# Performance work log

Measured on AMD Instinct MI355X. Metric: run time of the kernel, lower is better.

Reference implementation:

```python
import jax, jax.numpy as jnp
import numpy as np

SQRT2 = 1.4142135623730951
MH_C = 0.8673250705840776  # (2/sqrt(3)) * pi**(-1/4), mexican-hat normalizer


def _bn(x, eps=1e-5):
    # BatchNorm (training-mode batch stats, default affine gamma=1, beta=0)
    mu = jnp.mean(x, axis=0, keepdims=True)
    var = jnp.var(x, axis=0, keepdims=True)
    return (x - mu) / jnp.sqrt(var + eps)


def setup_inputs() -> dict:
    key = jax.random.key(0)
    ks = jax.random.split(key, 10)
    N, F, E, B, OUT = 1024, 1024, 32768, 16, 10
    H = F // 2  # 512 after Haar DWT
    x = jax.random.normal(ks[0], (N, F), dtype=jnp.float32)
    edge_index = jax.random.randint(ks[1], (2, E), 0, N, dtype=jnp.int32)
    batch = jnp.sort(jax.random.randint(ks[2], (N,), 0, B, dtype=jnp.int32))
    w_att = jax.random.normal(ks[3], (2,), dtype=jnp.float32)  # Linear(2,1,bias=False)
    wk_scale = jnp.ones((H, H), dtype=jnp.float32)
    wk_trans = jax.random.normal(ks[4], (H, H), dtype=jnp.float32) * 0.1
    wk_wav_w = jax.random.normal(ks[5], (H, H), dtype=jnp.float32) * 0.05
    wk_base_w = jax.random.normal(ks[6], (H, H), dtype=jnp.float32) * 0.05
    fc1_w = jax.random.normal(ks[7], (512, F + H), dtype=jnp.float32) * 0.02
    fc1_b = jnp.zeros((512,), dtype=jnp.float32)
    fc2_w = jax.random.normal(ks[8], (OUT, 512), dtype=jnp.float32) * 0.02
    fc2_b = jnp.zeros((OUT,), dtype=jnp.float32)
    return {"x": x, "w_att": w_att, "wk_scale": wk_scale, "wk_trans": wk_trans,
            "wk_wav_w": wk_wav_w, "wk_base_w": wk_base_w, "fc1_w": fc1_w,
            "fc1_b": fc1_b, "fc2_w": fc2_w, "fc2_b": fc2_b,
            "edge_index": edge_index, "batch": batch, "num_graphs": B}


def reference(x, w_att, wk_scale, wk_trans, wk_wav_w, wk_base_w,
              fc1_w, fc1_b, fc2_w, fc2_b, edge_index, batch, num_graphs):
    N = x.shape[0]
    # --- WaveletAttention: Haar ('db1') DWT over the feature dim ---
    xe, xo = x[:, 0::2], x[:, 1::2]
    low = (xe + xo) / SQRT2            # [N, 512]
    high = (xe - xo) / SQRT2           # [N, 512]
    scores = jax.nn.sigmoid(low * w_att[0] + high * w_att[1])
    h = scores * low + (1.0 - scores) * high
    # --- GINConv aggregation (eps=0): self + sum of neighbor features ---
    src, dst = edge_index[0], edge_index[1]
    agg = h + jax.ops.segment_sum(h[src], dst, num_segments=N)  # [N, 512]
    # --- WavKAN layer 512->512 (mexican hat) ---
    xs = (agg[:, None, :] - wk_trans) / wk_scale                # [N, 512, 512]
    xs2 = xs * xs
    mh = MH_C * (1.0 - xs2) * jnp.exp(-0.5 * xs2)
    wav = jnp.einsum('noi,oi->no', mh, wk_wav_w)                # [N, 512]
    base = jax.nn.silu(agg) @ wk_base_w.T
    conv_out = _bn(wav + base)   # WavKAN-internal BatchNorm1d
    conv_out = _bn(conv_out)     # bn1 (dropout p=0 -> identity)
    # --- skip concat + bn2 ---
    z = _bn(jnp.concatenate([x, conv_out], axis=1))             # [N, 1536]
    # --- global mean pool over graphs ---
    sums = jax.ops.segment_sum(z, batch, num_segments=num_graphs)
    cnts = jax.ops.segment_sum(jnp.ones((N,), z.dtype), batch, num_segments=num_graphs)
    pooled = sums / jnp.maximum(cnts, 1.0)[:, None]             # [B, 1536]
    # --- classifier head (eval-mode dropout = identity) ---
    h1 = jax.nn.relu(pooled @ fc1_w.T + fc1_b)
    return h1 @ fc2_w.T + fc2_b
```

## Files before the change

kernel.cpp:

```cpp
#include <hip/hip_runtime.h>
#include <math.h>

#define N_NODES 1024
#define F_DIM   1024
#define H_DIM   512
#define E_EDGES 32768
#define B_GRAPHS 16
#define OUT_DIM 10
#define FH_DIM  1536
#define EPS 1e-5f
#define MH_C_D 0.8673250705840776
#define C2_D   0.72134752044448170368
#define C2_F   ((float)C2_D)
#define CSC    0.84932180028801904272f
#define WC2F   ((float)(MH_C_D / C2_D))
#define INV_SQRT2 0.70710678118654752440f

typedef float v2f __attribute__((ext_vector_type(2)));
typedef unsigned int u32;
typedef const __attribute__((address_space(1))) u32 gu32;
typedef __attribute__((address_space(3))) u32 lu32;

#if __has_builtin(__builtin_amdgcn_exp2f)
#define EXP2NEG(x) __builtin_amdgcn_exp2f(-(x))
#else
#define EXP2NEG(x) __expf(-0.69314718055994530942f * (x))
#endif

__global__ __launch_bounds__(256) void k_setup(const float* __restrict__ x,
                                               const float* __restrict__ watt,
                                               float* __restrict__ h,
                                               const float* __restrict__ scale,
                                               const float* __restrict__ trans,
                                               const float* __restrict__ ww,
                                               const float* __restrict__ bw,
                                               float* __restrict__ pk,
                                               float* __restrict__ zbase) {
    const int bid = blockIdx.x;
    const int t = threadIdx.x;
    if (bid < 2048) {
        int idx = bid * 256 + t;
        float2 p = ((const float2*)x)[idx];
        float lo = (p.x + p.y) * INV_SQRT2;
        float hi = (p.x - p.y) * INV_SQRT2;
        float tt = lo * watt[0] + hi * watt[1];
        float sc = 1.0f / (1.0f + __expf(-tt));
        h[idx] = sc * lo + (1.0f - sc) * hi;
    } else if (bid < 3072) {
        int g = (bid - 2048) * 256 + t;
        float iv = 1.0f / scale[g];
        float4 p;
        p.x = iv * CSC;
        p.y = trans[g] * iv * CSC;
        p.z = ww[g] * WC2F;
        p.w = bw[g];
        ((float4*)pk)[g] = p;
    } else {
        zbase[(bid - 3072) * 256 + t] = 0.0f;
    }
}

__global__ __launch_bounds__(256) void k_hx(const int* __restrict__ dst,
                                            int* __restrict__ deg,
                                            const float* __restrict__ x,
                                            float* __restrict__ xsum,
                                            float* __restrict__ xsum2) {
    const int bid = blockIdx.x;
    const int t = threadIdx.x;
    if (bid < 128) {
        int e = bid * 256 + t;
        atomicAdd(&deg[dst[e]], 1);
    } else {
        const int n0 = (bid - 128) * 16;
        float s[4] = {}, s2[4] = {};
        for (int r = 0; r < 16; ++r) {
            #pragma unroll
            for (int ch = 0; ch < 4; ++ch) {
                float v = x[(n0 + r) * F_DIM + ch * 256 + t];
                s[ch] += v; s2[ch] += v * v;
            }
        }
        #pragma unroll
        for (int ch = 0; ch < 4; ++ch) {
            unsafeAtomicAdd(&xsum[ch * 256 + t], s[ch]);
            unsafeAtomicAdd(&xsum2[ch * 256 + t], s2[ch]);
        }
    }
}

__global__ __launch_bounds__(1024) void k_scan(const int* __restrict__ deg,
                                               int* __restrict__ start,
                                               int* __restrict__ cursor) {
    __shared__ int wsum[16];
    int t = threadIdx.x;
    int lane = t & 63, wid = t >> 6;
    int v = deg[t];
    int x = v;
    #pragma unroll
    for (int off = 1; off < 64; off <<= 1) {
        int y = __shfl_up(x, off, 64);
        if (lane >= off) x += y;
    }
    if (lane == 63) wsum[wid] = x;
    __syncthreads();
    if (t < 16) {
        int w = wsum[t];
        int xs = w;
        #pragma unroll
        for (int off = 1; off < 16; off <<= 1) {
            int y = __shfl_up(xs, off, 64);
            if (t >= off) xs += y;
        }
        wsum[t] = xs - w;
    }
    __syncthreads();
    int excl = wsum[wid] + x - v;
    start[t] = excl;
    cursor[t] = excl;
}

__global__ __launch_bounds__(256) void k_fill(const int* __restrict__ src,
                                              const int* __restrict__ dst,
                                              int* __restrict__ cursor,
                                              int* __restrict__ elist) {
    int e = blockIdx.x * 256 + threadIdx.x;
    int slot = atomicAdd(&cursor[dst[e]], 1);
    elist[slot] = src[e];
}

__global__ __launch_bounds__(256) void k_gather(const float* __restrict__ h,
                                                const int* __restrict__ start,
                                                const int* __restrict__ deg,
                                                const int* __restrict__ elist,
                                                float* __restrict__ agg) {
    int d = blockIdx.x;
    int t = threadIdx.x;
    int st = start[d], dg = deg[d];
    const float2* h2 = (const float2*)h;
    float2 a = h2[d * 256 + t];
    int k = 0;
    for (; k + 4 <= dg; k += 4) {
        int s0 = elist[st + k];
        int s1 = elist[st + k + 1];
        int s2 = elist[st + k + 2];
        int s3 = elist[st + k + 3];
        float2 v0 = h2[s0 * 256 + t];
        float2 v1 = h2[s1 * 256 + t];
        float2 v2 = h2[s2 * 256 + t];
        float2 v3 = h2[s3 * 256 + t];
        a.x += (v0.x + v1.x) + (v2.x + v3.x);
        a.y += (v0.y + v1.y) + (v2.y + v3.y);
    }
    for (; k < dg; ++k) {
        int s0 = elist[st + k];
        float2 v0 = h2[s0 * 256 + t];
        a.x += v0.x; a.y += v0.y;
    }
    ((float2*)agg)[d * 256 + t] = a;
}

__global__ __launch_bounds__(256) void k_transpose(const float* __restrict__ agg,
                                                   float* __restrict__ aggT,
                                                   float* __restrict__ siluT) {
    __shared__ float tile[64 * 65];
    const int t = threadIdx.x;
    const int n0 = blockIdx.x * 64;
    const int i0 = blockIdx.y * 64;
    #pragma unroll
    for (int v = 0; v < 4; ++v) {
        int flat = v * 256 + t;
        int r = flat >> 4, c4 = flat & 15;
        float4 a = *(const float4*)&agg[(n0 + r) * H_DIM + i0 + c4 * 4];
        tile[(c4 * 4 + 0) * 65 + r] = a.x;
        tile[(c4 * 4 + 1) * 65 + r] = a.y;
        tile[(c4 * 4 + 2) * 65 + r] = a.z;
        tile[(c4 * 4 + 3) * 65 + r] = a.w;
    }
    __syncthreads();
    #pragma unroll
    for (int v = 0; v < 4; ++v) {
        int flat = v * 256 + t;
        int il = flat >> 4, c4 = flat & 15;
        float4 a;
        a.x = tile[il * 65 + c4 * 4 + 0];
        a.y = tile[il * 65 + c4 * 4 + 1];
        a.z = tile[il * 65 + c4 * 4 + 2];
        a.w = tile[il * 65 + c4 * 4 + 3];
        int g = (i0 + il) * N_NODES + n0 + c4 * 4;
        *(float4*)&aggT[g] = a;
        float4 s;
        s.x = a.x / (1.0f + __expf(-a.x));
        s.y = a.y / (1.0f + __expf(-a.y));
        s.z = a.z / (1.0f + __expf(-a.z));
        s.w = a.w / (1.0f + __expf(-a.w));
        *(float4*)&siluT[g] = s;
    }
}

#define TN 64
#define TO 64
#define KI 16
#define TOP (TO + 1)
#define ZSPLIT 8
#define ZLEN (H_DIM / ZSPLIT)
__global__ __launch_bounds__(256) void k_wavelet(const float* __restrict__ aggT,
                                                 const float* __restrict__ siluT,
                                                 const float* __restrict__ pk,
                                                 float* __restrict__ vbp) {
    __shared__ float sA[KI * TN];
    __shared__ float sS[KI * TN];
    __shared__ float4 sP4[KI * TOP];

    const int t  = threadIdx.x;
    const int n0 = blockIdx.x * TN;
    const int o0 = blockIdx.y * TO;
    const int z0 = blockIdx.z * ZLEN;
    const int nl = (t & 15) * 4;
    const int ol = (t >> 4) * 4;

    v2f accw[4][2] = {};
    v2f accb[4][2] = {};

    for (int stg = 0; stg < ZLEN / KI; ++stg) {
        const int i0 = z0 + stg * KI;
        __syncthreads();
        {
            int g = (i0 + (t >> 4)) * N_NODES + n0 + nl;
            __builtin_amdgcn_global_load_lds((gu32*)&aggT[g],  (lu32*)&sA[t * 4], 16, 0, 0);
            __builtin_amdgcn_global_load_lds((gu32*)&siluT[g], (lu32*)&sS[t * 4], 16, 0, 0);
        }
        #pragma unroll
        for (int j = 0; j < 4; ++j) {
            int u = j * 256 + t;
            int o = u >> 4, ii = u & 15;
            sP4[ii * TOP + o] = ((const float4*)pk)[(o0 + o) * H_DIM + i0 + ii];
        }
        __syncthreads();
        #pragma unroll 4
        for (int ii = 0; ii < KI; ++ii) {
            float4 a = *(const float4*)&sA[ii * TN + nl];
            float4 s = *(const float4*)&sS[ii * TN + nl];
            v2f a01 = {a.x, a.y}, a23 = {a.z, a.w};
            v2f s01 = {s.x, s.y}, s23 = {s.z, s.w};
            #pragma unroll
            for (int oo = 0; oo < 4; ++oo) {
                float4 p = sP4[ii * TOP + ol + oo];
                float wcs = p.z * C2_F;
                v2f iv2 = {p.x, p.x};
                v2f tf2 = {p.y, p.y};
                v2f w2  = {p.z, p.z};
                v2f wc2 = {wcs, wcs};
                v2f b2  = {p.w, p.w};
                {
                    v2f y  = a01 * iv2 - tf2;
                    v2f y2 = y * y;
                    v2f e; e.x = EXP2NEG(y2.x); e.y = EXP2NEG(y2.y);
                    v2f wm = wc2 - w2 * y2;
                    accw[oo][0] += wm * e;
                    accb[oo][0] += s01 * b2;
                }
                {
                    v2f y  = a23 * iv2 - tf2;
                    v2f y2 = y * y;
                    v2f e; e.x = EXP2NEG(y2.x); e.y = EXP2NEG(y2.y);
                    v2f wm = wc2 - w2 * y2;
                    accw[oo][1] += wm * e;
                    accb[oo][1] += s23 * b2;
                }
            }
        }
    }
    float* out = vbp + (size_t)blockIdx.z * (N_NODES * H_DIM);
    #pragma unroll
    for (int nn = 0; nn < 4; ++nn) {
        int pr = nn >> 1, cmu = nn & 1;
        float4 o4;
        o4.x = cmu ? accw[0][pr].y + accb[0][pr].y : accw[0][pr].x + accb[0][pr].x;
        o4.y = cmu ? accw[1][pr].y + accb[1][pr].y : accw[1][pr].x + accb[1][pr].x;
        o4.z = cmu ? accw[2][pr].y + accb[2][pr].y : accw[2][pr].x + accb[2][pr].x;
        o4.w = cmu ? accw[3][pr].y + accb[3][pr].y : accw[3][pr].x + accb[3][pr].x;
        *(float4*)&out[(n0 + nl + nn) * H_DIM + o0 + ol] = o4;
    }
}

__global__ __launch_bounds__(256) void k_reduce(const float* __restrict__ vbp,
                                                float* __restrict__ vb,
                                                float* __restrict__ colsum,
                                                float* __restrict__ colsum2) {
    const int b = blockIdx.x;
    const int o0 = (b & 7) * 64;
    const int n0 = (b >> 3) * 64;
    const int t = threadIdx.x;
    const int oc = o0 + (t & 63);
    const int nsub = t >> 6;
    float s = 0.f, s2 = 0.f;
    for (int r = 0; r < 16; ++r) {
        int n = n0 + r * 4 + nsub;
        size_t idx = (size_t)n * H_DIM + oc;
        float v = 0.f;
        #pragma unroll
        for (int z = 0; z < ZSPLIT; ++z) v += vbp[z * (N_NODES * H_DIM) + idx];
        vb[idx] = v;
        s += v; s2 += v * v;
    }
    __shared__ float sh1[256], sh2[256];
    sh1[t] = s; sh2[t] = s2;
    __syncthreads();
    if (t < 64) {
        s  = sh1[t] + sh1[t + 64] + sh1[t + 128] + sh1[t + 192];
        s2 = sh2[t] + sh2[t + 64] + sh2[t + 128] + sh2[t + 192];
        unsafeAtomicAdd(&colsum[o0 + t], s);
        unsafeAtomicAdd(&colsum2[o0 + t], s2);
    }
}

__global__ __launch_bounds__(256) void k_pool(const float* __restrict__ x,
                                              const float* __restrict__ vb,
                                              const int* __restrict__ batch,
                                              const float* __restrict__ colsum,
                                              const float* __restrict__ colsum2,
                                              const float* __restrict__ xsum,
                                              const float* __restrict__ xsum2,
                                              float* __restrict__ pooled) {
    const int b = blockIdx.x;
    const int ch = blockIdx.y;
    const int t = threadIdx.x;

    __shared__ int s_cnt[4];
    __shared__ int s_st;
    int c = 0;
    for (int n = t; n < N_NODES; n += 256) {
        int bb = batch[n];
        int pb = (n == 0) ? -1 : batch[n - 1];
        c += (bb == b) ? 1 : 0;
        if (bb == b && pb != b) s_st = n;
    }
    #pragma unroll
    for (int off = 32; off > 0; off >>= 1) c += __shfl_down(c, off);
    if ((t & 63) == 0) s_cnt[t >> 6] = c;
    __syncthreads();
    int cnt = s_cnt[0] + s_cnt[1] + s_cnt[2] + s_cnt[3];
    int st = (cnt > 0) ? s_st : 0;
    float ic = (cnt > 0) ? 1.0f / (float)cnt : 0.f;

    float acc = 0.f;
    if (ch < 4) {
        int col = ch * 256 + t;
        float mu  = xsum[col] * (1.0f / N_NODES);
        float var = xsum2[col] * (1.0f / N_NODES) - mu * mu;
        if (var < 0.f) var = 0.f;
        float S = 1.0f / sqrtf(var + EPS);
        const float* base = x + col;
        for (int r = 0; r < cnt; ++r) acc += base[(size_t)(st + r) * F_DIM];
        pooled[b * FH_DIM + col] = (acc * ic - mu) * S;
    } else {
        int col = (ch - 4) * 256 + t;
        float mu  = colsum[col] * (1.0f / N_NODES);
        float var = colsum2[col] * (1.0f / N_NODES) - mu * mu;
        if (var < 0.f) var = 0.f;
        float s1v = 1.0f / sqrtf(var + EPS);
        float v1  = var * s1v * s1v;
        float s2v = 1.0f / sqrtf(v1 + EPS);
        float v2  = v1 * s2v * s2v;
        float s3v = 1.0f / sqrtf(v2 + EPS);
        float S = s1v * s2v * s3v;
        const float* base = vb + col;
        for (int r = 0; r < cnt; ++r) acc += base[(size_t)(st + r) * H_DIM];
        pooled[b * FH_DIM + F_DIM + col] = (acc * ic - mu) * S;
    }
}

__global__ __launch_bounds__(256) void k_fc1(const float* __restrict__ pooled,
                                             const float* __restrict__ w,
                                             const float* __restrict__ bias,
                                             float* __restrict__ h1) {
    int wid = (blockIdx.x * 256 + threadIdx.x) >> 6;
    int lane = threadIdx.x & 63;
    int b = wid >> 9, o = wid & 511;
    const float4* pr = (const float4*)(pooled + b * FH_DIM);
    const float4* wr = (const float4*)(w + o * FH_DIM);
    float acc = 0.f;
    #pragma unroll
    for (int k = 0; k < 6; ++k) {
        float4 a = pr[k * 64 + lane];
        float4 v = wr[k * 64 + lane];
        acc += a.x * v.x + a.y * v.y + a.z * v.z + a.w * v.w;
    }
    #pragma unroll
    for (int off = 32; off > 0; off >>= 1) acc += __shfl_down(acc, off);
    if (lane == 0) h1[b * H_DIM + o] = fmaxf(acc + bias[o], 0.f);
}

__global__ __launch_bounds__(256) void k_fc2(const float* __restrict__ h1,
                                             const float* __restrict__ w,
                                             const float* __restrict__ bias,
                                             float* __restrict__ outp) {
    int wid = (blockIdx.x * 256 + threadIdx.x) >> 6;
    int lane = threadIdx.x & 63;
    if (wid >= B_GRAPHS * OUT_DIM) return;
    int b = wid / OUT_DIM, u = wid % OUT_DIM;
    const float4* hr = (const float4*)(h1 + b * H_DIM);
    const float4* wr = (const float4*)(w + u * H_DIM);
    float acc = 0.f;
    #pragma unroll
    for (int k = 0; k < 2; ++k) {
        float4 a = hr[k * 64 + lane];
        float4 v = wr[k * 64 + lane];
        acc += a.x * v.x + a.y * v.y + a.z * v.z + a.w * v.w;
    }
    #pragma unroll
    for (int off = 32; off > 0; off >>= 1) acc += __shfl_down(acc, off);
    if (lane == 0) outp[b * OUT_DIM + u] = acc + bias[u];
}

extern "C" void kernel_launch(void* const* d_in, const int* in_sizes, int n_in,
                              void* d_out, int out_size, void* d_ws, size_t ws_size,
                              hipStream_t stream) {
    const float* x       = (const float*)d_in[0];
    const float* w_att   = (const float*)d_in[1];
    const float* wk_scale= (const float*)d_in[2];
    const float* wk_trans= (const float*)d_in[3];
    const float* wk_wav  = (const float*)d_in[4];
    const float* wk_base = (const float*)d_in[5];
    const float* fc1_w   = (const float*)d_in[6];
    const float* fc1_b   = (const float*)d_in[7];
    const float* fc2_w   = (const float*)d_in[8];
    const float* fc2_b   = (const float*)d_in[9];
    const int*   eidx    = (const int*)d_in[10];
    const int*   batch   = (const int*)d_in[11];
    float* outp = (float*)d_out;

    float* ws = (float*)d_ws;
    const int NH = N_NODES * H_DIM;
    float* h      = ws;
    float* agg    = h + NH;
    float* aggT   = agg + NH;
    float* siluT  = aggT + NH;
    float* pk     = siluT + NH;
    float* vbp    = pk + 4 * (H_DIM * H_DIM);
    float* vb     = vbp + (size_t)ZSPLIT * NH;
    float* colsum = vb + NH;
    float* colsum2= colsum + 512;
    float* xsum   = colsum2 + 512;
    float* xsum2  = xsum + 1024;
    int*   deg    = (int*)(xsum2 + 1024);
    int*   estart = deg + N_NODES;
    int*   cursor = estart + N_NODES;
    int*   elist  = cursor + N_NODES;
    float* pooled = (float*)(elist + E_EDGES);
    float* h1     = pooled + B_GRAPHS * FH_DIM;

    const int* src = eidx;
    const int* dst = eidx + E_EDGES;

    k_setup<<<3088, 256, 0, stream>>>(x, w_att, h, wk_scale, wk_trans, wk_wav, wk_base,
                                      pk, colsum);
    k_hx<<<192, 256, 0, stream>>>(dst, deg, x, xsum, xsum2);
    k_scan<<<1, N_NODES, 0, stream>>>(deg, estart, cursor);
    k_fill<<<E_EDGES / 256, 256, 0, stream>>>(src, dst, cursor, elist);
    k_gather<<<N_NODES, 256, 0, stream>>>(h, estart, deg, elist, agg);
    {
        dim3 grid(N_NODES / 64, H_DIM / 64);
        k_transpose<<<grid, 256, 0, stream>>>(agg, aggT, siluT);
    }
    {
        dim3 grid(N_NODES / TN, H_DIM / TO, ZSPLIT);
        k_wavelet<<<grid, 256, 0, stream>>>(aggT, siluT, pk, vbp);
    }
    k_reduce<<<128, 256, 0, stream>>>(vbp, vb, colsum, colsum2);
    {
        dim3 grid(B_GRAPHS, 6);
        k_pool<<<grid, 256, 0, stream>>>(x, vb, batch, colsum, colsum2, xsum, xsum2, pooled);
    }
    k_fc1<<<(B_GRAPHS * H_DIM * 64) / 256, 256, 0, stream>>>(pooled, fc1_w, fc1_b, h1);
    k_fc2<<<(B_GRAPHS * OUT_DIM * 64 + 255) / 256, 256, 0, stream>>>(h1, fc2_w, fc2_b, outp);
}
```

Baseline: 195.2 us.

## Double-buffer wavelet LDS tiles, read params directly, use packed asm, fuse scan+fill

The wavelet kernel now double-buffers the aggT/siluT tiles in LDS, prefetching the next stage while computing the current one. It drops the per-stage shared-memory staging of the packed parameters and reads them straight from global memory per thread. The inner math is rewritten with inline v_pk_fma/v_pk_mul asm on pre-negated parameters to cut instruction count, with launch bounds set to 4 blocks per SM. Separately, the scan and edge-fill kernels are fused into one single-block kernel that uses LDS atomics, which removes a launch but serialises the 32K-edge fill onto one workgroup.

```diff
diff --git a/kernel.cpp b/kernel.cpp
--- a/kernel.cpp
+++ b/kernel.cpp
@@ -26,6 +26,18 @@
 #else
 #define EXP2NEG(x) __expf(-0.69314718055994530942f * (x))
 #endif
+
+#define PK_FMA_BB(d, a, p) \
+    asm("v_pk_fma_f32 %0, %1, %2, %2 op_sel:[0,0,1] op_sel_hi:[1,0,1]" \
+        : "=v"(d) : "v"(a), "v"(p))
+#define PK_MUL2(d, a, b) \
+    asm("v_pk_mul_f32 %0, %1, %2" : "=v"(d) : "v"(a), "v"(b))
+#define PK_WZC(d, s, k) \
+    asm("v_pk_mul_f32 %0, %1, %2 op_sel:[0,0] op_sel_hi:[0,1]" \
+        : "=v"(d) : "v"(s), "v"(k))
+#define PK_FMA_HI_ACC(acc, s, p) \
+    asm("v_pk_fma_f32 %0, %1, %2, %0 op_sel:[0,1,0] op_sel_hi:[1,1,1]" \
+        : "+v"(acc) : "v"(s), "v"(p))
 
 __global__ __launch_bounds__(256) void k_setup(const float* __restrict__ x,
                                                const float* __restrict__ watt,
@@ -51,8 +63,8 @@
         float iv = 1.0f / scale[g];
         float4 p;
         p.x = iv * CSC;
-        p.y = trans[g] * iv * CSC;
-        p.z = ww[g] * WC2F;
+        p.y = -(trans[g] * iv * CSC);
+        p.z = -(ww[g] * WC2F);
         p.w = bw[g];
         ((float4*)pk)[g] = p;
     } else {
@@ -88,10 +100,13 @@
     }
 }
 
-__global__ __launch_bounds__(1024) void k_scan(const int* __restrict__ deg,
-                                               int* __restrict__ start,
-                                               int* __restrict__ cursor) {
+__global__ __launch_bounds__(1024) void k_scanfill(const int* __restrict__ deg,
+                                                   const int* __restrict__ src,
+                                                   const int* __restrict__ dst,
+                                                   int* __restrict__ start,
+                                                   int* __restrict__ elist) {
     __shared__ int wsum[16];
+    __shared__ int scur[N_NODES];
     int t = threadIdx.x;
     int lane = t & 63, wid = t >> 6;
     int v = deg[t];
@@ -116,16 +131,15 @@
     __syncthreads();
     int excl = wsum[wid] + x - v;
     start[t] = excl;
-    cursor[t] = excl;
-}
-
-__global__ __launch_bounds__(256) void k_fill(const int* __restrict__ src,
-                                              const int* __restrict__ dst,
-                                              int* __restrict__ cursor,
-                                              int* __restrict__ elist) {
-    int e = blockIdx.x * 256 + threadIdx.x;
-    int slot = atomicAdd(&cursor[dst[e]], 1);
-    elist[slot] = src[e];
+    scur[t] = excl;
+    __syncthreads();
+    #pragma unroll
+    for (int r = 0; r < E_EDGES / 1024; ++r) {
+        int e = r * 1024 + t;
+        int d = dst[e];
+        int slot = atomicAdd(&scur[d], 1);
+        elist[slot] = src[e];
+    }
 }
 
 __global__ __launch_bounds__(256) void k_gather(const float* __restrict__ h,
@@ -200,16 +214,15 @@
 #define TN 64
 #define TO 64
 #define KI 16
-#define TOP (TO + 1)
 #define ZSPLIT 8
 #define ZLEN (H_DIM / ZSPLIT)
-__global__ __launch_bounds__(256) void k_wavelet(const float* __restrict__ aggT,
-                                                 const float* __restrict__ siluT,
-                                                 const float* __restrict__ pk,
-                                                 float* __restrict__ vbp) {
-    __shared__ float sA[KI * TN];
-    __shared__ float sS[KI * TN];
-    __shared__ float4 sP4[KI * TOP];
+#define NSTG (ZLEN / KI)
+__global__ __launch_bounds__(256, 4) void k_wavelet(const float* __restrict__ aggT,
+                                                    const float* __restrict__ siluT,
+                                                    const float* __restrict__ pk,
+                                                    float* __restrict__ vbp) {
+    __shared__ float sA[2][KI * TN];
+    __shared__ float sS[2][KI * TN];
 
     const int t  = threadIdx.x;
     const int n0 = blockIdx.x * TN;
@@ -220,55 +233,58 @@
 
     v2f accw[4][2] = {};
     v2f accb[4][2] = {};
-
-    for (int stg = 0; stg < ZLEN / KI; ++stg) {
+    v2f kC2; kC2.x = 1.0f; kC2.y = -C2_F;
+
+    const v2f* prow0 = (const v2f*)pk + (size_t)(o0 + ol) * (H_DIM * 2);
+
+    {
+        int g = (z0 + (t >> 4)) * N_NODES + n0 + nl;
+        __builtin_amdgcn_global_load_lds((gu32*)&aggT[g],  (lu32*)&sA[0][t * 4], 16, 0, 0);
+        __builtin_amdgcn_global_load_lds((gu32*)&siluT[g], (lu32*)&sS[0][t * 4], 16, 0, 0);
+    }
+    __syncthreads();
+
+    #pragma unroll
+    for (int stg = 0; stg < NSTG; ++stg) {
         const int i0 = z0 + stg * KI;
-        __syncthreads();
-        {
-            int g = (i0 + (t >> 4)) * N_NODES + n0 + nl;
-            __builtin_amdgcn_global_load_lds((gu32*)&aggT[g],  (lu32*)&sA[t * 4], 16, 0, 0);
-            __builtin_amdgcn_global_load_lds((gu32*)&siluT[g], (lu32*)&sS[t * 4], 16, 0, 0);
+        if (stg + 1 < NSTG) {
+            int g = (i0 + KI + (t >> 4)) * N_NODES + n0 + nl;
+            __builtin_amdgcn_global_load_lds((gu32*)&aggT[g],
+                                             (lu32*)&sA[(stg + 1) & 1][t * 4], 16, 0, 0);
+            __builtin_amdgcn_global_load_lds((gu32*)&siluT[g],
+                                             (lu32*)&sS[(stg + 1) & 1][t * 4], 16, 0, 0);
         }
-        #pragma unroll
-        for (int j = 0; j < 4; ++j) {
-            int u = j * 256 + t;
-            int o = u >> 4, ii = u & 15;
-            sP4[ii * TOP + o] = ((const float4*)pk)[(o0 + o) * H_DIM + i0 + ii];
+        const float* pA = sA[stg & 1];
+        const float* pS = sS[stg & 1];
+        #pragma unroll 4
+        for (int ii = 0; ii < KI; ++ii) {
+            v2f a01 = *(const v2f*)&pA[ii * TN + nl];
+            v2f a23 = *(const v2f*)&pA[ii * TN + nl + 2];
+            v2f s01 = *(const v2f*)&pS[ii * TN + nl];
+            v2f s23 = *(const v2f*)&pS[ii * TN + nl + 2];
+            #pragma unroll
+            for (int oo = 0; oo < 4; ++oo) {
+                const v2f* pp = prow0 + ((size_t)oo * H_DIM + (i0 + ii)) * 2;
+                v2f pxy = pp[0];
+                v2f pzw = pp[1];
+                v2f wzc; PK_WZC(wzc, pzw, kC2);
+                v2f y0;  PK_FMA_BB(y0, a01, pxy);
+                v2f y1;  PK_FMA_BB(y1, a23, pxy);
+                v2f q0;  PK_MUL2(q0, y0, y0);
+                v2f q1;  PK_MUL2(q1, y1, y1);
+                v2f w0;  PK_FMA_BB(w0, q0, wzc);
+                v2f w1;  PK_FMA_BB(w1, q1, wzc);
+                float e00 = EXP2NEG(q0.x), e01 = EXP2NEG(q0.y);
+                float e10 = EXP2NEG(q1.x), e11 = EXP2NEG(q1.y);
+                accw[oo][0].x += w0.x * e00;
+                accw[oo][0].y += w0.y * e01;
+                accw[oo][1].x += w1.x * e10;
+                accw[oo][1].y += w1.y * e11;
+                PK_FMA_HI_ACC(accb[oo][0], s01, pzw);
+                PK_FMA_HI_ACC(accb[oo][1], s23, pzw);
+            }
         }
         __syncthreads();
-        #pragma unroll 4
-        for (int ii = 0; ii < KI; ++ii) {
-            float4 a = *(const float4*)&sA[ii * TN + nl];
-            float4 s = *(const float4*)&sS[ii * TN + nl];
-            v2f a01 = {a.x, a.y}, a23 = {a.z, a.w};
-            v2f s01 = {s.x, s.y}, s23 = {s.z, s.w};
-            #pragma unroll
-            for (int oo = 0; oo < 4; ++oo) {
-                float4 p = sP4[ii * TOP + ol + oo];
-                float wcs = p.z * C2_F;
-                v2f iv2 = {p.x, p.x};
-                v2f tf2 = {p.y, p.y};
-                v2f w2  = {p.z, p.z};
-                v2f wc2 = {wcs, wcs};
-                v2f b2  = {p.w, p.w};
-                {
-                    v2f y  = a01 * iv2 - tf2;
-                    v2f y2 = y * y;
-                    v2f e; e.x = EXP2NEG(y2.x); e.y = EXP2NEG(y2.y);
-                    v2f wm = wc2 - w2 * y2;
-                    accw[oo][0] += wm * e;
-                    accb[oo][0] += s01 * b2;
-                }
-                {
-                    v2f y  = a23 * iv2 - tf2;
-                    v2f y2 = y * y;
-                    v2f e; e.x = EXP2NEG(y2.x); e.y = EXP2NEG(y2.y);
-                    v2f wm = wc2 - w2 * y2;
-                    accw[oo][1] += wm * e;
-                    accb[oo][1] += s23 * b2;
-                }
-            }
-        }
     }
     float* out = vbp + (size_t)blockIdx.z * (N_NODES * H_DIM);
     #pragma unroll
@@ -445,8 +461,7 @@
     float* xsum2  = xsum + 1024;
     int*   deg    = (int*)(xsum2 + 1024);
     int*   estart = deg + N_NODES;
-    int*   cursor = estart + N_NODES;
-    int*   elist  = cursor + N_NODES;
+    int*   elist  = estart + N_NODES;
     float* pooled = (float*)(elist + E_EDGES);
     float* h1     = pooled + B_GRAPHS * FH_DIM;
 
@@ -456,8 +471,7 @@
     k_setup<<<3088, 256, 0, stream>>>(x, w_att, h, wk_scale, wk_trans, wk_wav, wk_base,
                                       pk, colsum);
     k_hx<<<192, 256, 0, stream>>>(dst, deg, x, xsum, xsum2);
-    k_scan<<<1, N_NODES, 0, stream>>>(deg, estart, cursor);
-    k_fill<<<E_EDGES / 256, 256, 0, stream>>>(src, dst, cursor, elist);
+    k_scanfill<<<1, 1024, 0, stream>>>(deg, src, dst, estart, elist);
     k_gather<<<N_NODES, 256, 0, stream>>>(h, estart, deg, elist, agg);
     {
         dim3 grid(N_NODES / 64, H_DIM / 64);
```

Measured after the change: 237.5 us. +21.6%, slower.

## Split base matmul out, double-buffer wavelet tiles, atomically accumulate split-K results

Applied to the files above, without the earlier changes.

The base (silu) matmul moves out of the wavelet kernel into a separate tiled GEMM, which removes the siluT buffer and its extra traffic. The wavelet kernel now double-buffers its LDS tiles and uses an 8x2 per-thread register tile with hand-written packed FMA instructions. Pre-negated constants drop a few ops per element. Split-K partials are accumulated into vb with float atomics instead of writing 8 partial buffers and reducing them, and a separate stats kernel computes the column sums. This trades the partial-buffer round trip for many atomic updates and floating-point summation whose order varies between runs.

```diff
diff --git a/kernel.cpp b/kernel.cpp
--- a/kernel.cpp
+++ b/kernel.cpp
@@ -14,6 +14,7 @@
 #define C2_F   ((float)C2_D)
 #define CSC    0.84932180028801904272f
 #define WC2F   ((float)(MH_C_D / C2_D))
+#define MH_C_F ((float)MH_C_D)
 #define INV_SQRT2 0.70710678118654752440f
 
 typedef float v2f __attribute__((ext_vector_type(2)));
@@ -26,6 +27,12 @@
 #else
 #define EXP2NEG(x) __expf(-0.69314718055994530942f * (x))
 #endif
+
+#define PK_FMA_BB(d, a, p) \
+    asm("v_pk_fma_f32 %0, %1, %2, %2 op_sel:[0,0,1] op_sel_hi:[1,0,1]" \
+        : "=v"(d) : "v"(a), "v"(p))
+#define PK_MUL2(d, a, b) \
+    asm("v_pk_mul_f32 %0, %1, %2" : "=v"(d) : "v"(a), "v"(b))
 
 __global__ __launch_bounds__(256) void k_setup(const float* __restrict__ x,
                                                const float* __restrict__ watt,
@@ -33,9 +40,9 @@
                                                const float* __restrict__ scale,
                                                const float* __restrict__ trans,
                                                const float* __restrict__ ww,
-                                               const float* __restrict__ bw,
                                                float* __restrict__ pk,
-                                               float* __restrict__ zbase) {
+                                               float* __restrict__ zbase,
+                                               float* __restrict__ vb) {
     const int bid = blockIdx.x;
     const int t = threadIdx.x;
     if (bid < 2048) {
@@ -49,14 +56,17 @@
     } else if (bid < 3072) {
         int g = (bid - 2048) * 256 + t;
         float iv = 1.0f / scale[g];
+        float wwv = ww[g];
         float4 p;
         p.x = iv * CSC;
-        p.y = trans[g] * iv * CSC;
-        p.z = ww[g] * WC2F;
-        p.w = bw[g];
+        p.y = -(trans[g] * iv * CSC);
+        p.z = -(wwv * WC2F);
+        p.w = wwv * MH_C_F;
         ((float4*)pk)[g] = p;
+    } else if (bid < 3088) {
+        zbase[(bid - 3072) * 256 + t] = 0.0f;
     } else {
-        zbase[(bid - 3072) * 256 + t] = 0.0f;
+        vb[(bid - 3088) * 256 + t] = 0.0f;
     }
 }
 
@@ -160,8 +170,7 @@
 }
 
 __global__ __launch_bounds__(256) void k_transpose(const float* __restrict__ agg,
-                                                   float* __restrict__ aggT,
-                                                   float* __restrict__ siluT) {
+                                                   float* __restrict__ aggT) {
     __shared__ float tile[64 * 65];
     const int t = threadIdx.x;
     const int n0 = blockIdx.x * 64;
@@ -186,131 +195,167 @@
         a.y = tile[il * 65 + c4 * 4 + 1];
         a.z = tile[il * 65 + c4 * 4 + 2];
         a.w = tile[il * 65 + c4 * 4 + 3];
-        int g = (i0 + il) * N_NODES + n0 + c4 * 4;
-        *(float4*)&aggT[g] = a;
-        float4 s;
-        s.x = a.x / (1.0f + __expf(-a.x));
-        s.y = a.y / (1.0f + __expf(-a.y));
-        s.z = a.z / (1.0f + __expf(-a.z));
-        s.w = a.w / (1.0f + __expf(-a.w));
-        *(float4*)&siluT[g] = s;
+        *(float4*)&aggT[(i0 + il) * N_NODES + n0 + c4 * 4] = a;
     }
 }
 
 #define TN 64
 #define TO 64
 #define KI 16
-#define TOP (TO + 1)
 #define ZSPLIT 8
 #define ZLEN (H_DIM / ZSPLIT)
+#define NSTG (ZLEN / KI)
 __global__ __launch_bounds__(256) void k_wavelet(const float* __restrict__ aggT,
-                                                 const float* __restrict__ siluT,
                                                  const float* __restrict__ pk,
-                                                 float* __restrict__ vbp) {
-    __shared__ float sA[KI * TN];
-    __shared__ float sS[KI * TN];
-    __shared__ float4 sP4[KI * TOP];
+                                                 float* __restrict__ vb) {
+    __shared__ float  sA[2][KI * TN];
+    __shared__ float4 sP[2][KI * TO];
 
     const int t  = threadIdx.x;
     const int n0 = blockIdx.x * TN;
     const int o0 = blockIdx.y * TO;
     const int z0 = blockIdx.z * ZLEN;
-    const int nl = (t & 15) * 4;
-    const int ol = (t >> 4) * 4;
-
-    v2f accw[4][2] = {};
-    v2f accb[4][2] = {};
-
-    for (int stg = 0; stg < ZLEN / KI; ++stg) {
+    const int nb8 = (t & 7) * 8;
+    const int og  = t >> 3;
+    const int ob2 = og * 2;
+
+    const int srow = t >> 4, scol4 = (t & 15) * 4;
+    const int pio = t >> 4, pic = t & 15;
+    const float4* pk4 = (const float4*)pk;
+
+    v2f accw[2][4] = {};
+
+    {
+        int g = (z0 + srow) * N_NODES + n0 + scol4;
+        __builtin_amdgcn_global_load_lds((gu32*)&aggT[g], (lu32*)&sA[0][t * 4], 16, 0, 0);
+        float4 pr[4];
+        #pragma unroll
+        for (int j = 0; j < 4; ++j)
+            pr[j] = pk4[(size_t)(o0 + j * 16 + pio) * H_DIM + z0 + pic];
+        #pragma unroll
+        for (int j = 0; j < 4; ++j)
+            sP[0][pic * TO + j * 16 + pio] = pr[j];
+    }
+    __syncthreads();
+
+    for (int stg = 0; stg < NSTG; ++stg) {
         const int i0 = z0 + stg * KI;
+        const int nb = (stg + 1) & 1;
+        float4 pr[4];
+        if (stg + 1 < NSTG) {
+            int g = (i0 + KI + srow) * N_NODES + n0 + scol4;
+            __builtin_amdgcn_global_load_lds((gu32*)&aggT[g], (lu32*)&sA[nb][t * 4], 16, 0, 0);
+            #pragma unroll
+            for (int j = 0; j < 4; ++j)
+                pr[j] = pk4[(size_t)(o0 + j * 16 + pio) * H_DIM + i0 + KI + pic];
+        }
+        const float*  pA = sA[stg & 1];
+        const float4* pP = sP[stg & 1];
+        #pragma unroll
+        for (int ii = 0; ii < KI; ++ii) {
+            const float4 af0 = *(const float4*)&pA[ii * TN + nb8];
+            const float4 af1 = *(const float4*)&pA[ii * TN + nb8 + 4];
+            v2f a01 = {af0.x, af0.y}, a23 = {af0.z, af0.w};
+            v2f a45 = {af1.x, af1.y}, a67 = {af1.z, af1.w};
+            #pragma unroll
+            for (int oo = 0; oo < 2; ++oo) {
+                float4 pq = pP[ii * TO + ob2 + oo];
+                v2f pxy = {pq.x, pq.y};
+                v2f pzw = {pq.z, pq.w};
+                v2f y0, y1, y2, y3, q0, q1, q2, q3, w0, w1, w2, w3;
+                PK_FMA_BB(y0, a01, pxy); PK_FMA_BB(y1, a23, pxy);
+                PK_FMA_BB(y2, a45, pxy); PK_FMA_BB(y3, a67, pxy);
+                PK_MUL2(q0, y0, y0); PK_MUL2(q1, y1, y1);
+                PK_MUL2(q2, y2, y2); PK_MUL2(q3, y3, y3);
+                PK_FMA_BB(w0, q0, pzw); PK_FMA_BB(w1, q1, pzw);
+                PK_FMA_BB(w2, q2, pzw); PK_FMA_BB(w3, q3, pzw);
+                accw[oo][0].x += w0.x * EXP2NEG(q0.x);
+                accw[oo][0].y += w0.y * EXP2NEG(q0.y);
+                accw[oo][1].x += w1.x * EXP2NEG(q1.x);
+                accw[oo][1].y += w1.y * EXP2NEG(q1.y);
+                accw[oo][2].x += w2.x * EXP2NEG(q2.x);
+                accw[oo][2].y += w2.y * EXP2NEG(q2.y);
+                accw[oo][3].x += w3.x * EXP2NEG(q3.x);
+                accw[oo][3].y += w3.y * EXP2NEG(q3.y);
+            }
+        }
+        if (stg + 1 < NSTG) {
+            #pragma unroll
+            for (int j = 0; j < 4; ++j)
+                sP[nb][pic * TO + j * 16 + pio] = pr[j];
+        }
+        __syncthreads();
+    }
+    const int oc = o0 + ob2;
+    #pragma unroll
+    for (int p = 0; p < 4; ++p) {
+        int ne = n0 + nb8 + 2 * p;
+        unsafeAtomicAdd(&vb[(size_t)ne * H_DIM + oc],           accw[0][p].x);
+        unsafeAtomicAdd(&vb[(size_t)ne * H_DIM + oc + 1],       accw[1][p].x);
+        unsafeAtomicAdd(&vb[(size_t)(ne + 1) * H_DIM + oc],     accw[0][p].y);
+        unsafeAtomicAdd(&vb[(size_t)(ne + 1) * H_DIM + oc + 1], accw[1][p].y);
+    }
+}
+
+__global__ __launch_bounds__(256) void k_base(const float* __restrict__ aggT,
+                                              const float* __restrict__ bw,
+                                              float* __restrict__ vb) {
+    __shared__ float sA[16][32];
+    __shared__ float sB[16][33];
+    const int t = threadIdx.x;
+    const int n0 = blockIdx.x * 32, o0 = blockIdx.y * 32;
+    const int nl = (t & 15) * 2, ol = (t >> 4) * 2;
+    float acc[2][2] = {};
+    for (int ic = 0; ic < 32; ++ic) {
+        int i0 = ic * 16;
         __syncthreads();
         {
-            int g = (i0 + (t >> 4)) * N_NODES + n0 + nl;
-            __builtin_amdgcn_global_load_lds((gu32*)&aggT[g],  (lu32*)&sA[t * 4], 16, 0, 0);
-            __builtin_amdgcn_global_load_lds((gu32*)&siluT[g], (lu32*)&sS[t * 4], 16, 0, 0);
-        }
-        #pragma unroll
-        for (int j = 0; j < 4; ++j) {
-            int u = j * 256 + t;
-            int o = u >> 4, ii = u & 15;
-            sP4[ii * TOP + o] = ((const float4*)pk)[(o0 + o) * H_DIM + i0 + ii];
+            int flat = t * 2;
+            int r = flat >> 5, c = flat & 31;
+            float2 av = *(const float2*)&aggT[(i0 + r) * N_NODES + n0 + c];
+            sA[r][c]     = av.x / (1.0f + __expf(-av.x));
+            sA[r][c + 1] = av.y / (1.0f + __expf(-av.y));
+            int ob = t >> 3, iq = (t & 7) * 2;
+            float2 bv = *(const float2*)&bw[(o0 + ob) * H_DIM + i0 + iq];
+            sB[iq][ob]     = bv.x;
+            sB[iq + 1][ob] = bv.y;
         }
         __syncthreads();
-        #pragma unroll 4
-        for (int ii = 0; ii < KI; ++ii) {
-            float4 a = *(const float4*)&sA[ii * TN + nl];
-            float4 s = *(const float4*)&sS[ii * TN + nl];
-            v2f a01 = {a.x, a.y}, a23 = {a.z, a.w};
-            v2f s01 = {s.x, s.y}, s23 = {s.z, s.w};
-            #pragma unroll
-            for (int oo = 0; oo < 4; ++oo) {
-                float4 p = sP4[ii * TOP + ol + oo];
-                float wcs = p.z * C2_F;
-                v2f iv2 = {p.x, p.x};
-                v2f tf2 = {p.y, p.y};
-                v2f w2  = {p.z, p.z};
-                v2f wc2 = {wcs, wcs};
-                v2f b2  = {p.w, p.w};
-                {
-                    v2f y  = a01 * iv2 - tf2;
-                    v2f y2 = y * y;
-                    v2f e; e.x = EXP2NEG(y2.x); e.y = EXP2NEG(y2.y);
-                    v2f wm = wc2 - w2 * y2;
-                    accw[oo][0] += wm * e;
-                    accb[oo][0] += s01 * b2;
-                }
-                {
-                    v2f y  = a23 * iv2 - tf2;
-                    v2f y2 = y * y;
-                    v2f e; e.x = EXP2NEG(y2.x); e.y = EXP2NEG(y2.y);
-                    v2f wm = wc2 - w2 * y2;
-                    accw[oo][1] += wm * e;
-                    accb[oo][1] += s23 * b2;
-                }
-            }
-        }
-    }
-    float* out = vbp + (size_t)blockIdx.z * (N_NODES * H_DIM);
-    #pragma unroll
-    for (int nn = 0; nn < 4; ++nn) {
-        int pr = nn >> 1, cmu = nn & 1;
-        float4 o4;
-        o4.x = cmu ? accw[0][pr].y + accb[0][pr].y : accw[0][pr].x + accb[0][pr].x;
-        o4.y = cmu ? accw[1][pr].y + accb[1][pr].y : accw[1][pr].x + accb[1][pr].x;
-        o4.z = cmu ? accw[2][pr].y + accb[2][pr].y : accw[2][pr].x + accb[2][pr].x;
-        o4.w = cmu ? accw[3][pr].y + accb[3][pr].y : accw[3][pr].x + accb[3][pr].x;
-        *(float4*)&out[(n0 + nl + nn) * H_DIM + o0 + ol] = o4;
-    }
-}
-
-__global__ __launch_bounds__(256) void k_reduce(const float* __restrict__ vbp,
-                                                float* __restrict__ vb,
-                                                float* __restrict__ colsum,
-                                                float* __restrict__ colsum2) {
-    const int b = blockIdx.x;
-    const int o0 = (b & 7) * 64;
-    const int n0 = (b >> 3) * 64;
+        #pragma unroll
+        for (int ii = 0; ii < 16; ++ii) {
+            float a0 = sA[ii][nl], a1 = sA[ii][nl + 1];
+            float b0 = sB[ii][ol], b1 = sB[ii][ol + 1];
+            acc[0][0] += a0 * b0; acc[0][1] += a0 * b1;
+            acc[1][0] += a1 * b0; acc[1][1] += a1 * b1;
+        }
+    }
+    #pragma unroll
+    for (int j = 0; j < 2; ++j)
+        #pragma unroll
+        for (int k = 0; k < 2; ++k)
+            unsafeAtomicAdd(&vb[(size_t)(n0 + nl + j) * H_DIM + o0 + ol + k], acc[j][k]);
+}
+
+__global__ __launch_bounds__(256) void k_stats(const float* __restrict__ vb,
+                                               float* __restrict__ colsum,
+                                               float* __restrict__ colsum2) {
     const int t = threadIdx.x;
-    const int oc = o0 + (t & 63);
-    const int nsub = t >> 6;
+    const int c = blockIdx.x * 32 + (t & 31);
+    const int p = t >> 5;
     float s = 0.f, s2 = 0.f;
-    for (int r = 0; r < 16; ++r) {
-        int n = n0 + r * 4 + nsub;
-        size_t idx = (size_t)n * H_DIM + oc;
-        float v = 0.f;
-        #pragma unroll
-        for (int z = 0; z < ZSPLIT; ++z) v += vbp[z * (N_NODES * H_DIM) + idx];
-        vb[idx] = v;
+    for (int r = 0; r < 128; ++r) {
+        float v = vb[(size_t)(p * 128 + r) * H_DIM + c];
         s += v; s2 += v * v;
     }
     __shared__ float sh1[256], sh2[256];
     sh1[t] = s; sh2[t] = s2;
     __syncthreads();
-    if (t < 64) {
-        s  = sh1[t] + sh1[t + 64] + sh1[t + 128] + sh1[t + 192];
-        s2 = sh2[t] + sh2[t + 64] + sh2[t + 128] + sh2[t + 192];
-        unsafeAtomicAdd(&colsum[o0 + t], s);
-        unsafeAtomicAdd(&colsum2[o0 + t], s2);
+    if (t < 32) {
+        float a = 0.f, a2 = 0.f;
+        #pragma unroll
+        for (int q = 0; q < 8; ++q) { a += sh1[q * 32 + t]; a2 += sh2[q * 32 + t]; }
+        colsum[blockIdx.x * 32 + t]  = a;
+        colsum2[blockIdx.x * 32 + t] = a2;
     }
 }
 
@@ -435,10 +480,8 @@
     float* h      = ws;
     float* agg    = h + NH;
     float* aggT   = agg + NH;
-    float* siluT  = aggT + NH;
-    float* pk     = siluT + NH;
-    float* vbp    = pk + 4 * (H_DIM * H_DIM);
-    float* vb     = vbp + (size_t)ZSPLIT * NH;
+    float* pk     = aggT + NH;
+    float* vb     = pk + 4 * (H_DIM * H_DIM);
     float* colsum = vb + NH;
     float* colsum2= colsum + 512;
     float* xsum   = colsum2 + 512;
@@ -453,21 +496,25 @@
     const int* src = eidx;
     const int* dst = eidx + E_EDGES;
 
-    k_setup<<<3088, 256, 0, stream>>>(x, w_att, h, wk_scale, wk_trans, wk_wav, wk_base,
-                                      pk, colsum);
+    k_setup<<<5136, 256, 0, stream>>>(x, w_att, h, wk_scale, wk_trans, wk_wav,
+                                      pk, colsum, vb);
     k_hx<<<192, 256, 0, stream>>>(dst, deg, x, xsum, xsum2);
     k_scan<<<1, N_NODES, 0, stream>>>(deg, estart, cursor);
     k_fill<<<E_EDGES / 256, 256, 0, stream>>>(src, dst, cursor, elist);
     k_gather<<<N_NODES, 256, 0, stream>>>(h, estart, deg, elist, agg);
     {
         dim3 grid(N_NODES / 64, H_DIM / 64);
-        k_transpose<<<grid, 256, 0, stream>>>(agg, aggT, siluT);
+        k_transpose<<<grid, 256, 0, stream>>>(agg, aggT);
+    }
+    {
+        dim3 grid(N_NODES / 32, H_DIM / 32);
+        k_base<<<grid, 256, 0, stream>>>(aggT, wk_base, vb);
     }
     {
         dim3 grid(N_NODES / TN, H_DIM / TO, ZSPLIT);
-        k_wavelet<<<grid, 256, 0, stream>>>(aggT, siluT, pk, vbp);
-    }
-    k_reduce<<<128, 256, 0, stream>>>(vbp, vb, colsum, colsum2);
+        k_wavelet<<<grid, 256, 0, stream>>>(aggT, pk, vb);
+    }
+    k_stats<<<16, 256, 0, stream>>>(vb, colsum, colsum2);
     {
         dim3 grid(B_GRAPHS, 6);
         k_pool<<<grid, 256, 0, stream>>>(x, vb, batch, colsum, colsum2, xsum, xsum2, pooled);
```

Result: slower. 310.7 us (+59.1%).
